# Kernel tuning notes

Hardware: AMD Instinct MI355X
Metric: run time of the kernel (lower is better)

Reference implementation:

```python
import jax, jax.numpy as jnp
import numpy as np

# HP constants (mirroring the torch module's HP)
NUM_EFFECTIVE_QUEUES = 2
DISCOUNT_FACTOR = 0.995
USE_MIN_FOR_LOSS_REDUCE = False
ENTROPY_COEF = 0.0  # entropy branch disabled, matching HP.ENTROPY_COEF = 0.0

N_CLAUSES = 50000
FEAT_DIM = 64
HIDDEN = 256
KEY_DIM = 256
T_SEL = 1000  # number of SEL events in the journal
NEG_INF = -1e30


def setup_inputs() -> dict:
    key = jax.random.key(0)
    ks = jax.random.split(key, 10)
    feature_vecs = jax.random.normal(ks[0], (N_CLAUSES, FEAT_DIM), dtype=jnp.float32)
    W1 = jax.random.normal(ks[1], (FEAT_DIM, HIDDEN), dtype=jnp.float32) / np.sqrt(FEAT_DIM)
    b1 = jnp.zeros((HIDDEN,), dtype=jnp.float32)
    W2 = jax.random.normal(ks[2], (HIDDEN, KEY_DIM), dtype=jnp.float32) / np.sqrt(HIDDEN)
    b2 = jnp.zeros((KEY_DIM,), dtype=jnp.float32)
    keys_W = jax.random.normal(ks[3], (NUM_EFFECTIVE_QUEUES, KEY_DIM), dtype=jnp.float32) / np.sqrt(KEY_DIM)
    # Per-SEL-event passive set (equivalent to replaying ADD/REM events host-side):
    passive_mask = jax.random.uniform(ks[4], (T_SEL, N_CLAUSES)) < 0.10
    # proof_flas membership per clause, good = passive & proof
    proof = jax.random.uniform(ks[5], (N_CLAUSES,)) < 0.05
    good_mask = passive_mask & proof[None, :]
    # queue index = time % NUM_EFFECTIVE_QUEUES, time increments per SEL event
    queue_idx = jnp.arange(T_SEL, dtype=jnp.int32) % NUM_EFFECTIVE_QUEUES
    return {
        "feature_vecs": feature_vecs, "W1": W1, "b1": b1, "W2": W2, "b2": b2,
        "keys_W": keys_W, "passive_mask": passive_mask, "good_mask": good_mask,
        "queue_idx": queue_idx,
    }


def reference(feature_vecs, W1, b1, W2, b2, keys_W, passive_mask, good_mask, queue_idx):
    # clause_embedder: 2-layer MLP
    h = jax.nn.relu(feature_vecs @ W1 + b1)         # [N, H]
    emb = h @ W2 + b2                                # [N, K]
    logits = keys_W @ emb.T                          # [Q, N]
    ev_logits = logits[queue_idx]                    # [T, N] gather per SEL event

    num_good = good_mask.sum(axis=-1)                # [T]
    num_pass = passive_mask.sum(axis=-1)             # [T]
    num_bad = num_pass - num_good
    valid = (num_good > 0) & (num_bad > 0)           # events contributing loss

    # log_softmax restricted to the passive set
    masked = jnp.where(passive_mask, ev_logits, NEG_INF)
    lsm = jax.nn.log_softmax(masked, axis=-1)        # [T, N]

    # cross_entropy = -mean(lsm over good idxs)  (USE_MIN_FOR_LOSS_REDUCE = False)
    good_sum = jnp.where(good_mask, lsm, 0.0).sum(axis=-1)
    ce = -good_sum / jnp.maximum(num_good, 1).astype(lsm.dtype)

    # factor *= DISCOUNT_FACTOR after each counted step
    steps_before = (jnp.cumsum(valid.astype(jnp.int32)) - valid.astype(jnp.int32))
    factor = jnp.asarray(DISCOUNT_FACTOR, lsm.dtype) ** steps_before.astype(lsm.dtype)

    weight = factor * (num_bad.astype(lsm.dtype) / jnp.maximum(num_pass, 1).astype(lsm.dtype))
    loss_terms = jnp.where(valid, weight * ce, 0.0)
    steps = valid.sum().astype(lsm.dtype)
    loss = loss_terms.sum() / jnp.maximum(steps, 1.0)
    return loss.reshape(1)
```

## Files before the change

### kernel.cpp

```cpp
#include <hip/hip_runtime.h>
#include <hip/hip_bf16.h>

#define N_CL   50000
#define FEAT   64
#define HID    256
#define KD     256
#define T_SEL  1000
#define NBLK   782
#define JSPLIT 4

#define NQUAD  12500
#define NCHUNK 20
#define CHUNKQ 625
#define GEV    5
#define SLOTS  10
#define LASTW  49

#define WK_OFF   0
#define CK_OFF   512
#define MQ_OFF   514
#define P_OFF    520
#define LG_OFF   (P_OFF + JSPLIT * 2 * N_CL)
#define CTAB_OFF 520
#define ACC_OFF  (CTAB_OFF + 100000)

__device__ __forceinline__ unsigned fkey(float f) {
    unsigned u = __float_as_uint(f);
    return (u & 0x80000000u) ? ~u : (u | 0x80000000u);
}
__device__ __forceinline__ float finv(unsigned k) {
    unsigned u = (k & 0x80000000u) ? (k ^ 0x80000000u) : ~k;
    return __uint_as_float(u);
}
__device__ __forceinline__ unsigned short f2bf(float f) {
    unsigned u = __float_as_uint(f);
    return (unsigned short)((u + 0x7FFFu + ((u >> 16) & 1u)) >> 16);
}
__device__ __forceinline__ float eLO(unsigned u) {
    return __uint_as_float(u << 16);
}
__device__ __forceinline__ float lHI(unsigned u) {
    return __uint_as_float(u & 0xFFFF0000u);
}

__global__ __launch_bounds__(256) void prep_kernel(
        const float* __restrict__ W2, const float* __restrict__ b2,
        const float* __restrict__ keysW,
        float* __restrict__ wk, float* __restrict__ ck,
        unsigned* __restrict__ mq) {
    __shared__ float sk0[KD], sk1[KD], sb2[KD], red[256];
    int tid = threadIdx.x;
    sk0[tid] = keysW[tid];
    sk1[tid] = keysW[KD + tid];
    sb2[tid] = b2[tid];
    if (tid < 2) mq[tid] = 0u;
    __syncthreads();

    const float* w2r = W2 + (size_t)tid * KD;
    float a0 = 0.f, a1 = 0.f;
    #pragma unroll 4
    for (int k = 0; k < KD; k++) {
        float w = w2r[k];
        a0 = fmaf(w, sk0[k], a0);
        a1 = fmaf(w, sk1[k], a1);
    }
    wk[tid * 2 + 0] = a0;
    wk[tid * 2 + 1] = a1;

    red[tid] = sk0[tid] * sb2[tid];
    __syncthreads();
    for (int s = 128; s > 0; s >>= 1) { if (tid < s) red[tid] += red[tid + s]; __syncthreads(); }
    if (tid == 0) ck[0] = red[0];
    __syncthreads();
    red[tid] = sk1[tid] * sb2[tid];
    __syncthreads();
    for (int s = 128; s > 0; s >>= 1) { if (tid < s) red[tid] += red[tid + s]; __syncthreads(); }
    if (tid == 0) ck[1] = red[0];
}

__global__ __launch_bounds__(64, 2) void mlp_kernel(
        const float* __restrict__ X, const float* __restrict__ W1,
        const float* __restrict__ b1, const float* __restrict__ wk,
        float* __restrict__ P) {
    int nb = blockIdx.x >> 2;
    int p  = blockIdx.x & 3;
    int n  = nb * 64 + threadIdx.x;
    int nc = (n < N_CL) ? n : (N_CL - 1);

    float x[FEAT];
    const float4* xp = (const float4*)(X + (size_t)nc * FEAT);
    #pragma unroll
    for (int k4 = 0; k4 < FEAT / 4; k4++) {
        float4 v = xp[k4];
        x[4 * k4 + 0] = v.x; x[4 * k4 + 1] = v.y;
        x[4 * k4 + 2] = v.z; x[4 * k4 + 3] = v.w;
    }

    float l0 = 0.f, l1 = 0.f;
    int j0 = p * 64;
    for (int jg = 0; jg < 64; jg += 16) {
        float h[16];
        #pragma unroll
        for (int u = 0; u < 16; u++) h[u] = b1[j0 + jg + u];
        #pragma unroll
        for (int k = 0; k < FEAT; k++) {
            const float* w1r = W1 + (size_t)k * HID + j0 + jg;
            float xv = x[k];
            #pragma unroll
            for (int u = 0; u < 16; u++) h[u] = fmaf(xv, w1r[u], h[u]);
        }
        #pragma unroll
        for (int u = 0; u < 16; u++) {
            float hv = fmaxf(h[u], 0.0f);
            l0 = fmaf(hv, wk[(j0 + jg + u) * 2 + 0], l0);
            l1 = fmaf(hv, wk[(j0 + jg + u) * 2 + 1], l1);
        }
    }
    if (n < N_CL) {
        P[((size_t)p * 2 + 0) * N_CL + n] = l0;
        P[((size_t)p * 2 + 1) * N_CL + n] = l1;
    }
}

__global__ __launch_bounds__(256) void logits_fin(
        const float* __restrict__ P, const float* __restrict__ ck,
        float* __restrict__ lg, unsigned* __restrict__ mq) {
    int n = blockIdx.x * 256 + threadIdx.x;
    float m0 = -1e30f, m1 = -1e30f;
    if (n < N_CL) {
        float l0 = ck[0], l1 = ck[1];
        #pragma unroll
        for (int p = 0; p < JSPLIT; p++) {
            l0 += P[((size_t)p * 2 + 0) * N_CL + n];
            l1 += P[((size_t)p * 2 + 1) * N_CL + n];
        }
        lg[n]        = l0;
        lg[N_CL + n] = l1;
        m0 = l0; m1 = l1;
    }
    for (int off = 32; off; off >>= 1) {
        m0 = fmaxf(m0, __shfl_xor(m0, off));
        m1 = fmaxf(m1, __shfl_xor(m1, off));
    }
    __shared__ float sm0[4], sm1[4];
    int w = threadIdx.x >> 6;
    if ((threadIdx.x & 63) == 0) { sm0[w] = m0; sm1[w] = m1; }
    __syncthreads();
    if (threadIdx.x == 0) {
        m0 = fmaxf(fmaxf(sm0[0], sm0[1]), fmaxf(sm0[2], sm0[3]));
        m1 = fmaxf(fmaxf(sm1[0], sm1[1]), fmaxf(sm1[2], sm1[3]));
        atomicMax(mq + 0, fkey(m0));
        atomicMax(mq + 1, fkey(m1));
    }
}

__global__ __launch_bounds__(256) void epack_kernel(
        const float* __restrict__ lg, const unsigned* __restrict__ mq,
        uint4* __restrict__ ctab) {
    int quad = blockIdx.x * 256 + threadIdx.x;
    if (quad >= NQUAD) return;
    #pragma unroll
    for (int q = 0; q < 2; q++) {
        float4 f = ((const float4*)lg)[(size_t)q * NQUAD + quad];
        float M = finv(mq[q]);
        uint4 cv;
        cv.x = ((unsigned)f2bf(f.x) << 16) | f2bf(__expf(f.x - M));
        cv.y = ((unsigned)f2bf(f.y) << 16) | f2bf(__expf(f.y - M));
        cv.z = ((unsigned)f2bf(f.z) << 16) | f2bf(__expf(f.z - M));
        cv.w = ((unsigned)f2bf(f.w) << 16) | f2bf(__expf(f.w - M));
        ctab[(size_t)q * NQUAD + quad] = cv;
    }
}

__global__ __launch_bounds__(64) void emain_kernel(
        const int* __restrict__ pass, const int* __restrict__ good,
        const int* __restrict__ qidx, const uint4* __restrict__ ctab,
        float4* __restrict__ acc) {
    int bid  = blockIdx.x;
    int c    = bid % NCHUNK;
    int rest = bid / NCHUNK;
    int par  = rest & 1;
    int grp  = rest >> 1;
    int lane = threadIdx.x;

    int t0 = par + 2 * (grp * GEV);
    int q  = qidx[t0] & 1;

    __shared__ uint4 ct[CHUNKQ];
    for (int i = lane; i < CHUNKQ; i += 64)
        ct[i] = ctab[(size_t)q * NQUAD + c * CHUNKQ + i];
    __syncthreads();

    int idx[SLOTS];
    #pragma unroll
    for (int s = 0; s < SLOTS; s++) {
        int i = s * 64 + lane;
        idx[s] = (i < CHUNKQ) ? i : (CHUNKQ - 1);
    }
    bool lastok = lane < LASTW;

    #pragma unroll
    for (int e = 0; e < GEV; e++) {
        int t = t0 + 2 * e;
        const int4* pb = (const int4*)pass + (size_t)t * NQUAD + c * CHUNKQ;
        const int4* gb = (const int4*)good + (size_t)t * NQUAD + c * CHUNKQ;

        int4 pm[SLOTS], gm[SLOTS];
        #pragma unroll
        for (int s = 0; s < SLOTS; s++) pm[s] = pb[idx[s]];
        #pragma unroll
        for (int s = 0; s < SLOTS; s++) gm[s] = gb[idx[s]];

        float sa = 0.f, sga = 0.f;
        int np = 0, ng = 0;
        #pragma unroll
        for (int s = 0; s < SLOTS; s++) {
            uint4 cv = ct[idx[s]];
            int4 p = pm[s], g = gm[s];
            if (s == SLOTS - 1 && !lastok) {
                p = make_int4(0, 0, 0, 0);
                g = make_int4(0, 0, 0, 0);
            }
            np += p.x + p.y + p.z + p.w;
            ng += g.x + g.y + g.z + g.w;
            sa  += p.x ? eLO(cv.x) : 0.0f;
            sa  += p.y ? eLO(cv.y) : 0.0f;
            sa  += p.z ? eLO(cv.z) : 0.0f;
            sa  += p.w ? eLO(cv.w) : 0.0f;
            sga += g.x ? lHI(cv.x) : 0.0f;
            sga += g.y ? lHI(cv.y) : 0.0f;
            sga += g.z ? lHI(cv.z) : 0.0f;
            sga += g.w ? lHI(cv.w) : 0.0f;
        }
        for (int off = 32; off; off >>= 1) {
            sa  += __shfl_xor(sa, off);
            sga += __shfl_xor(sga, off);
            np  += __shfl_xor(np, off);
            ng  += __shfl_xor(ng, off);
        }
        if (lane == 0)
            acc[(size_t)t * NCHUNK + c] =
                make_float4(sa, sga, (float)np, (float)ng);
    }
}

__global__ __launch_bounds__(1024) void final_kernel(
        const int* __restrict__ qidx, const float4* __restrict__ acc,
        const unsigned* __restrict__ mq, float* __restrict__ out) {
    int t = threadIdx.x;
    float s = 0.f, sg = 0.f, np = 0.f, ng = 0.f;
    int q = 0;
    if (t < T_SEL) {
        #pragma unroll 4
        for (int c = 0; c < NCHUNK; c++) {
            float4 a = acc[(size_t)t * NCHUNK + c];
            s += a.x; sg += a.y; np += a.z; ng += a.w;
        }
        q = qidx[t] & 1;
    }
    float M  = finv(mq[q]);
    float nb = np - ng;
    int valid = (t < T_SEL) && (ng > 0.5f) && (nb > 0.5f);

    __shared__ int sc[1024];
    sc[t] = valid;
    __syncthreads();
    for (int off = 1; off < 1024; off <<= 1) {
        int v = (t >= off) ? sc[t - off] : 0;
        __syncthreads();
        sc[t] += v;
        __syncthreads();
    }
    int sb    = sc[t] - valid;
    int steps = sc[1023];

    float ce   = logf(s) + M - sg / fmaxf(ng, 1.0f);
    float wgt  = powf(0.995f, (float)sb) * nb / fmaxf(np, 1.0f);
    float term = valid ? wgt * ce : 0.0f;

    __shared__ float sf[1024];
    sf[t] = term;
    __syncthreads();
    for (int off = 512; off; off >>= 1) {
        if (t < off) sf[t] += sf[t + off];
        __syncthreads();
    }
    if (t == 0) out[0] = sf[0] / fmaxf((float)steps, 1.0f);
}

extern "C" void kernel_launch(void* const* d_in, const int* in_sizes, int n_in,
                              void* d_out, int out_size, void* d_ws, size_t ws_size,
                              hipStream_t stream) {
    const float* X     = (const float*)d_in[0];
    const float* W1    = (const float*)d_in[1];
    const float* b1    = (const float*)d_in[2];
    const float* W2    = (const float*)d_in[3];
    const float* b2    = (const float*)d_in[4];
    const float* keysW = (const float*)d_in[5];
    const int*   pass  = (const int*)d_in[6];
    const int*   good  = (const int*)d_in[7];
    const int*   qidx  = (const int*)d_in[8];

    float*    ws   = (float*)d_ws;
    float*    wk   = ws + WK_OFF;
    float*    ck   = ws + CK_OFF;
    unsigned* mq   = (unsigned*)(ws + MQ_OFF);
    float*    P    = ws + P_OFF;
    float*    lg   = ws + LG_OFF;
    uint4*    ctab = (uint4*)(ws + CTAB_OFF);
    float4*   acc  = (float4*)(ws + ACC_OFF);
    float*    out  = (float*)d_out;

    hipLaunchKernelGGL(prep_kernel, dim3(1), dim3(256), 0, stream,
                       W2, b2, keysW, wk, ck, mq);
    hipLaunchKernelGGL(mlp_kernel, dim3(NBLK * JSPLIT), dim3(64), 0, stream,
                       X, W1, b1, wk, P);
    hipLaunchKernelGGL(logits_fin, dim3((N_CL + 255) / 256), dim3(256), 0, stream,
                       P, ck, lg, mq);
    hipLaunchKernelGGL(epack_kernel, dim3((NQUAD + 255) / 256), dim3(256), 0, stream,
                       lg, mq, ctab);
    hipLaunchKernelGGL(emain_kernel, dim3(NCHUNK * 200), dim3(64), 0, stream,
                       pass, good, qidx, ctab, acc);
    hipLaunchKernelGGL(final_kernel, dim3(1), dim3(1024), 0, stream,
                       qidx, acc, mq, out);
}
```

Before: 156.0 us.

## Pack passive and good masks into bitmasks before per-event reduction

Adds a streaming pack kernel that converts the int32 passive/good masks into 64-bit ballot bitmasks. A clause-permuted bf16 table is built so that each lane's bit lines up with its table entry. A new ebit kernel then reduces over the compact bitmasks, using popcount for the counts and shared-memory table lookups, with the work split into 14 column chunks per event. The full mask read still happens, but it moves into a simple bandwidth-bound kernel, at the cost of extra workspace and an added bitmask write/read pass. The new path runs only when the workspace is large enough; otherwise the old path is kept.

```diff
diff --git a/kernel.cpp b/kernel.cpp
--- a/kernel.cpp
+++ b/kernel.cpp
@@ -9,6 +9,13 @@
 #define NBLK   782
 #define JSPLIT 4
 
+#define WCH    196
+#define BPR    784
+#define CW     56
+#define NCH    14
+#define EPB    8
+#define GEB    63
+
 #define NQUAD  12500
 #define NCHUNK 20
 #define CHUNKQ 625
@@ -21,8 +28,13 @@
 #define MQ_OFF   514
 #define P_OFF    520
 #define LG_OFF   (P_OFF + JSPLIT * 2 * N_CL)
+#define PTAB_OFF 520
+#define ACCB_OFF 100880
+#define PB_OFF   (LG_OFF + 2 * N_CL)
+#define GB_OFF   (PB_OFF + 2 * T_SEL * BPR)
+#define WS_NEED  ((size_t)(GB_OFF + 2 * T_SEL * BPR) * 4)
 #define CTAB_OFF 520
-#define ACC_OFF  (CTAB_OFF + 100000)
+#define ACCO_OFF (CTAB_OFF + 100000)
 
 __device__ __forceinline__ unsigned fkey(float f) {
     unsigned u = __float_as_uint(f);
@@ -36,12 +48,8 @@
     unsigned u = __float_as_uint(f);
     return (unsigned short)((u + 0x7FFFu + ((u >> 16) & 1u)) >> 16);
 }
-__device__ __forceinline__ float eLO(unsigned u) {
-    return __uint_as_float(u << 16);
-}
-__device__ __forceinline__ float lHI(unsigned u) {
-    return __uint_as_float(u & 0xFFFF0000u);
-}
+__device__ __forceinline__ float eLO(unsigned u) { return __uint_as_float(u << 16); }
+__device__ __forceinline__ float lHI(unsigned u) { return __uint_as_float(u & 0xFFFF0000u); }
 
 __global__ __launch_bounds__(256) void prep_kernel(
         const float* __restrict__ W2, const float* __restrict__ b2,
@@ -152,6 +160,152 @@
         atomicMax(mq + 0, fkey(m0));
         atomicMax(mq + 1, fkey(m1));
     }
+}
+
+__global__ __launch_bounds__(256) void pack_kernel(
+        const int* __restrict__ pass, const int* __restrict__ good,
+        unsigned long long* __restrict__ pb, unsigned long long* __restrict__ gb) {
+    int item = blockIdx.x * 4 + (threadIdx.x >> 6);
+    int lane = threadIdx.x & 63;
+    int t  = item / WCH;
+    int wc = item - t * WCH;
+    if (t >= T_SEL) return;
+    int base = wc * 256 + lane * 4;
+    int4 pv = make_int4(0, 0, 0, 0), gv = make_int4(0, 0, 0, 0);
+    if (base + 3 < N_CL) {
+        pv = *(const int4*)(pass + (size_t)t * N_CL + base);
+        gv = *(const int4*)(good + (size_t)t * N_CL + base);
+    }
+    unsigned long long p0 = __ballot(pv.x), p1 = __ballot(pv.y);
+    unsigned long long p2 = __ballot(pv.z), p3 = __ballot(pv.w);
+    unsigned long long g0 = __ballot(gv.x), g1 = __ballot(gv.y);
+    unsigned long long g2 = __ballot(gv.z), g3 = __ballot(gv.w);
+    size_t o = (size_t)t * BPR + wc * 4;
+    if (lane == 0) { pb[o] = p0; pb[o + 1] = p1; pb[o + 2] = p2; pb[o + 3] = p3; }
+    else if (lane == 1) { gb[o] = g0; gb[o + 1] = g1; gb[o + 2] = g2; gb[o + 3] = g3; }
+}
+
+__global__ __launch_bounds__(256) void eperm_kernel(
+        const float* __restrict__ lg, const unsigned* __restrict__ mq,
+        unsigned* __restrict__ ptab) {
+    int i = blockIdx.x * 256 + threadIdx.x;
+    if (i >= 2 * BPR * 64) return;
+    int q = i / (BPR * 64);
+    int r = i - q * (BPR * 64);
+    int w = r >> 6, l = r & 63;
+    int clause = ((w >> 2) << 8) + l * 4 + (w & 3);
+    unsigned val = 0u;
+    if (clause < N_CL) {
+        float f = lg[q * N_CL + clause];
+        float M = finv(mq[q]);
+        val = ((unsigned)f2bf(f) << 16) | (unsigned)f2bf(__expf(f - M));
+    }
+    ptab[i] = val;
+}
+
+__global__ __launch_bounds__(256) void ebit_kernel(
+        const unsigned long long* __restrict__ pb,
+        const unsigned long long* __restrict__ gb,
+        const int* __restrict__ qidx, const unsigned* __restrict__ ptab,
+        float4* __restrict__ acc) {
+    int bid  = blockIdx.x;
+    int c    = bid % NCH;
+    int rest = bid / NCH;
+    int par  = rest & 1;
+    int g    = rest >> 1;
+    int tid  = threadIdx.x, wid = tid >> 6, lane = tid & 63;
+    int q    = qidx[par] & 1;
+
+    __shared__ unsigned pt[CW * 64];
+    __shared__ float4 red[4];
+    {
+        const uint4* src = (const uint4*)(ptab + (size_t)q * (BPR * 64) + c * (CW * 64));
+        for (int i = tid; i < CW * 64 / 4; i += 256)
+            ((uint4*)pt)[i] = src[i];
+    }
+    __syncthreads();
+
+    for (int e = 0; e < EPB; e++) {
+        int ev = g * EPB + e;
+        if (ev >= T_SEL / 2) break;
+        int t = par + 2 * ev;
+        const unsigned long long* pw = pb + (size_t)t * BPR + c * CW + wid * 14;
+        const unsigned long long* gw = gb + (size_t)t * BPR + c * CW + wid * 14;
+
+        float sa = 0.f, sga = 0.f;
+        int np = 0, ng = 0;
+        #pragma unroll
+        for (int k = 0; k < 14; k++) {
+            unsigned long long wv = pw[k];
+            np += (int)__popcll(wv);
+            unsigned v = pt[(wid * 14 + k) * 64 + lane];
+            if ((wv >> lane) & 1ull) sa += eLO(v);
+        }
+        #pragma unroll
+        for (int k = 0; k < 14; k++) {
+            unsigned long long wv = gw[k];
+            ng += (int)__popcll(wv);
+            unsigned v = pt[(wid * 14 + k) * 64 + lane];
+            if ((wv >> lane) & 1ull) sga += lHI(v);
+        }
+        for (int off = 32; off; off >>= 1) {
+            sa  += __shfl_xor(sa, off);
+            sga += __shfl_xor(sga, off);
+        }
+        if (lane == 0) red[wid] = make_float4(sa, sga, (float)np, (float)ng);
+        __syncthreads();
+        if (tid == 0) {
+            float4 a = red[0], b = red[1], cc = red[2], d = red[3];
+            acc[(size_t)t * NCH + c] = make_float4(
+                a.x + b.x + cc.x + d.x, a.y + b.y + cc.y + d.y,
+                a.z + b.z + cc.z + d.z, a.w + b.w + cc.w + d.w);
+        }
+        __syncthreads();
+    }
+}
+
+__global__ __launch_bounds__(1024) void final2_kernel(
+        const int* __restrict__ qidx, const float4* __restrict__ acc,
+        const unsigned* __restrict__ mq, float* __restrict__ out) {
+    int t = threadIdx.x;
+    float s = 0.f, sg = 0.f, np = 0.f, ng = 0.f;
+    int q = 0;
+    if (t < T_SEL) {
+        #pragma unroll 7
+        for (int c = 0; c < NCH; c++) {
+            float4 a = acc[(size_t)t * NCH + c];
+            s += a.x; sg += a.y; np += a.z; ng += a.w;
+        }
+        q = qidx[t] & 1;
+    }
+    float M  = finv(mq[q]);
+    float nb = np - ng;
+    int valid = (t < T_SEL) && (ng > 0.5f) && (nb > 0.5f);
+
+    __shared__ int sc[1024];
+    sc[t] = valid;
+    __syncthreads();
+    for (int off = 1; off < 1024; off <<= 1) {
+        int v = (t >= off) ? sc[t - off] : 0;
+        __syncthreads();
+        sc[t] += v;
+        __syncthreads();
+    }
+    int sb    = sc[t] - valid;
+    int steps = sc[1023];
+
+    float ce   = logf(s) + M - sg / fmaxf(ng, 1.0f);
+    float wgt  = powf(0.995f, (float)sb) * nb / fmaxf(np, 1.0f);
+    float term = valid ? wgt * ce : 0.0f;
+
+    __shared__ float sf[1024];
+    sf[t] = term;
+    __syncthreads();
+    for (int off = 512; off; off >>= 1) {
+        if (t < off) sf[t] += sf[t + off];
+        __syncthreads();
+    }
+    if (t == 0) out[0] = sf[0] / fmaxf((float)steps, 1.0f);
 }
 
 __global__ __launch_bounds__(256) void epack_kernel(
@@ -202,35 +356,35 @@
     #pragma unroll
     for (int e = 0; e < GEV; e++) {
         int t = t0 + 2 * e;
-        const int4* pb = (const int4*)pass + (size_t)t * NQUAD + c * CHUNKQ;
-        const int4* gb = (const int4*)good + (size_t)t * NQUAD + c * CHUNKQ;
+        const int4* pbm = (const int4*)pass + (size_t)t * NQUAD + c * CHUNKQ;
+        const int4* gbm = (const int4*)good + (size_t)t * NQUAD + c * CHUNKQ;
 
         int4 pm[SLOTS], gm[SLOTS];
         #pragma unroll
-        for (int s = 0; s < SLOTS; s++) pm[s] = pb[idx[s]];
-        #pragma unroll
-        for (int s = 0; s < SLOTS; s++) gm[s] = gb[idx[s]];
+        for (int s = 0; s < SLOTS; s++) pm[s] = pbm[idx[s]];
+        #pragma unroll
+        for (int s = 0; s < SLOTS; s++) gm[s] = gbm[idx[s]];
 
         float sa = 0.f, sga = 0.f;
         int np = 0, ng = 0;
         #pragma unroll
         for (int s = 0; s < SLOTS; s++) {
             uint4 cv = ct[idx[s]];
-            int4 p = pm[s], g = gm[s];
+            int4 p = pm[s], gmm = gm[s];
             if (s == SLOTS - 1 && !lastok) {
                 p = make_int4(0, 0, 0, 0);
-                g = make_int4(0, 0, 0, 0);
+                gmm = make_int4(0, 0, 0, 0);
             }
             np += p.x + p.y + p.z + p.w;
-            ng += g.x + g.y + g.z + g.w;
+            ng += gmm.x + gmm.y + gmm.z + gmm.w;
             sa  += p.x ? eLO(cv.x) : 0.0f;
             sa  += p.y ? eLO(cv.y) : 0.0f;
             sa  += p.z ? eLO(cv.z) : 0.0f;
             sa  += p.w ? eLO(cv.w) : 0.0f;
-            sga += g.x ? lHI(cv.x) : 0.0f;
-            sga += g.y ? lHI(cv.y) : 0.0f;
-            sga += g.z ? lHI(cv.z) : 0.0f;
-            sga += g.w ? lHI(cv.w) : 0.0f;
+            sga += gmm.x ? lHI(cv.x) : 0.0f;
+            sga += gmm.y ? lHI(cv.y) : 0.0f;
+            sga += gmm.z ? lHI(cv.z) : 0.0f;
+            sga += gmm.w ? lHI(cv.w) : 0.0f;
         }
         for (int off = 32; off; off >>= 1) {
             sa  += __shfl_xor(sa, off);
@@ -239,8 +393,7 @@
             ng  += __shfl_xor(ng, off);
         }
         if (lane == 0)
-            acc[(size_t)t * NCHUNK + c] =
-                make_float4(sa, sga, (float)np, (float)ng);
+            acc[(size_t)t * NCHUNK + c] = make_float4(sa, sga, (float)np, (float)ng);
     }
 }
 
@@ -301,26 +454,51 @@
     const int*   good  = (const int*)d_in[7];
     const int*   qidx  = (const int*)d_in[8];
 
-    float*    ws   = (float*)d_ws;
-    float*    wk   = ws + WK_OFF;
-    float*    ck   = ws + CK_OFF;
-    unsigned* mq   = (unsigned*)(ws + MQ_OFF);
-    float*    P    = ws + P_OFF;
-    float*    lg   = ws + LG_OFF;
-    uint4*    ctab = (uint4*)(ws + CTAB_OFF);
-    float4*   acc  = (float4*)(ws + ACC_OFF);
-    float*    out  = (float*)d_out;
-
-    hipLaunchKernelGGL(prep_kernel, dim3(1), dim3(256), 0, stream,
-                       W2, b2, keysW, wk, ck, mq);
-    hipLaunchKernelGGL(mlp_kernel, dim3(NBLK * JSPLIT), dim3(64), 0, stream,
-                       X, W1, b1, wk, P);
-    hipLaunchKernelGGL(logits_fin, dim3((N_CL + 255) / 256), dim3(256), 0, stream,
-                       P, ck, lg, mq);
-    hipLaunchKernelGGL(epack_kernel, dim3((NQUAD + 255) / 256), dim3(256), 0, stream,
-                       lg, mq, ctab);
-    hipLaunchKernelGGL(emain_kernel, dim3(NCHUNK * 200), dim3(64), 0, stream,
-                       pass, good, qidx, ctab, acc);
-    hipLaunchKernelGGL(final_kernel, dim3(1), dim3(1024), 0, stream,
-                       qidx, acc, mq, out);
-}
+    float*    ws = (float*)d_ws;
+    float*    wk = ws + WK_OFF;
+    float*    ck = ws + CK_OFF;
+    unsigned* mq = (unsigned*)(ws + MQ_OFF);
+    float*    P  = ws + P_OFF;
+    float*    lg = ws + LG_OFF;
+    float*    out = (float*)d_out;
+
+    bool big = (ws_size >= WS_NEED);
+
+    if (big) {
+        unsigned long long* pb = (unsigned long long*)(ws + PB_OFF);
+        unsigned long long* gb = (unsigned long long*)(ws + GB_OFF);
+        unsigned* ptab = (unsigned*)(ws + PTAB_OFF);
+        float4*   accb = (float4*)(ws + ACCB_OFF);
+
+        hipLaunchKernelGGL(pack_kernel, dim3((T_SEL * WCH) / 4), dim3(256), 0, stream,
+                           pass, good, pb, gb);
+        hipLaunchKernelGGL(prep_kernel, dim3(1), dim3(256), 0, stream,
+                           W2, b2, keysW, wk, ck, mq);
+        hipLaunchKernelGGL(mlp_kernel, dim3(NBLK * JSPLIT), dim3(64), 0, stream,
+                           X, W1, b1, wk, P);
+        hipLaunchKernelGGL(logits_fin, dim3((N_CL + 255) / 256), dim3(256), 0, stream,
+                           P, ck, lg, mq);
+        hipLaunchKernelGGL(eperm_kernel, dim3((2 * BPR * 64 + 255) / 256), dim3(256), 0, stream,
+                           lg, mq, (unsigned*)ptab);
+        hipLaunchKernelGGL(ebit_kernel, dim3(NCH * 2 * GEB), dim3(256), 0, stream,
+                           pb, gb, qidx, ptab, accb);
+        hipLaunchKernelGGL(final2_kernel, dim3(1), dim3(1024), 0, stream,
+                           qidx, accb, mq, out);
+    } else {
+        uint4*  ctab = (uint4*)(ws + CTAB_OFF);
+        float4* acco = (float4*)(ws + ACCO_OFF);
+
+        hipLaunchKernelGGL(prep_kernel, dim3(1), dim3(256), 0, stream,
+                           W2, b2, keysW, wk, ck, mq);
+        hipLaunchKernelGGL(mlp_kernel, dim3(NBLK * JSPLIT), dim3(64), 0, stream,
+                           X, W1, b1, wk, P);
+        hipLaunchKernelGGL(logits_fin, dim3((N_CL + 255) / 256), dim3(256), 0, stream,
+                           P, ck, lg, mq);
+        hipLaunchKernelGGL(epack_kernel, dim3((NQUAD + 255) / 256), dim3(256), 0, stream,
+                           lg, mq, ctab);
+        hipLaunchKernelGGL(emain_kernel, dim3(NCHUNK * 200), dim3(64), 0, stream,
+                           pass, good, qidx, ctab, acco);
+        hipLaunchKernelGGL(final_kernel, dim3(1), dim3(1024), 0, stream,
+                           qidx, acco, mq, out);
+    }
+}
```

Measured after the change: 246.8 us. +58.2%, slower.
